# Performance work log

Measured on AMD Instinct MI355X. Metric: run time of the kernel, lower is better.

The kernel has to match this reference:

```python
import jax, jax.numpy as jnp
import numpy as np

B, N, D = 16, 2048, 64


def setup_inputs() -> dict:
    key = jax.random.key(0)
    kq, kk, kv = jax.random.split(key, 3)
    queries = jax.random.normal(kq, (B, N, D), dtype=jnp.float32)
    keys = jax.random.normal(kk, (B, N, D), dtype=jnp.float32)
    values = jax.random.normal(kv, (B, N, D), dtype=jnp.float32)
    return {"queries": queries, "keys": keys, "values": values}


def reference(queries, keys, values):
    d = queries.shape[-1]
    scale = 1.0 / jnp.sqrt(jnp.asarray(d, dtype=queries.dtype))
    # scores: [B, N, N] = Q @ K^T / sqrt(d)
    scores = jnp.einsum("bqd,bkd->bqk", queries, keys) * scale
    attn = jax.nn.softmax(scores, axis=-1)
    # dropout prob = 0.0 -> identity (inference-faithful)
    out = jnp.einsum("bqk,bkd->bqd", attn, values)
    return out
```

## Files before the change

kernel.cpp:

```cpp
#include <hip/hip_runtime.h>

typedef __attribute__((ext_vector_type(8)))  __bf16 bf16x8;
typedef __attribute__((ext_vector_type(16))) float  f32x16;
typedef __attribute__((ext_vector_type(4)))  float  f32x4;

#define B_    16
#define N_    2048
#define D_    64
#define QBLK  128
#define KVBLK 32
#define NT    (N_ / KVBLK)
#define NG    4
#define TPG   (NT / NG)

#define VSTR    80
#define KSZ     4096
#define SLOT_SZ (KSZ + 64 * VSTR)
#define GRP_SZ  (2 * SLOT_SZ)
#define SMEM_SZ (NG * GRP_SZ)

static __device__ __forceinline__ float fast_exp2(float x) {
#if __has_builtin(__builtin_amdgcn_exp2f)
    return __builtin_amdgcn_exp2f(x);
#else
    return __expf(x * 0.6931471805599453f);
#endif
}

__global__ __attribute__((amdgpu_waves_per_eu(4, 4))) __launch_bounds__(1024)
void attn_fwd(const float* __restrict__ Qp, const float* __restrict__ Kp,
              const float* __restrict__ Vp, float* __restrict__ Op)
{
    __shared__ __align__(16) char smem[SMEM_SZ];

    const int tid  = threadIdx.x;
    const int g    = tid >> 8;
    const int tg   = tid & 255;
    const int lane = tid & 63;
    const int w    = (tid >> 6) & 3;
    const int h    = lane >> 5;
    const int qcol = lane & 31;

    const int bx    = blockIdx.x;
    const int batch = ((bx & 7) << 1) | ((bx >> 3) & 1);
    const int qtile = bx >> 4;
    const int q0w   = qtile * QBLK + w * 32;

    const float SL2E = 0.18033688011112042f;
    const size_t bboff = (size_t)batch * (N_ * D_);
    char* gbase = smem + g * GRP_SZ;

    const float* qrow = Qp + bboff + (size_t)(q0w + qcol) * D_ + h * 8;
    bf16x8 qf[4];
#pragma unroll
    for (int m = 0; m < 4; ++m) {
        f32x4 a = *reinterpret_cast<const f32x4*>(qrow + m * 16);
        f32x4 b = *reinterpret_cast<const f32x4*>(qrow + m * 16 + 4);
#pragma unroll
        for (int j = 0; j < 4; ++j) {
            qf[m][j]     = (__bf16)(a[j] * SL2E);
            qf[m][4 + j] = (__bf16)(b[j] * SL2E);
        }
    }

    const int krow = tg >> 3,  kcol = (tg & 7) * 8;
    const int vrow = tg & 31,  vcol = (tg >> 5) * 8;
    const int vin  = vrow & 15;
    const int vpos = ((vrow >> 4) * 2 + ((vin >> 2) & 1)) * 8 + (vin & 3) + 4 * (vin >> 3);
    const float* ksrc0 = Kp + bboff + (size_t)krow * D_ + kcol;
    const float* vsrc0 = Vp + bboff + (size_t)vrow * D_ + vcol;

    f32x4 kr[2], vr[2];
    auto load_tile = [&](int t) {
        const float* ks = ksrc0 + (size_t)t * KVBLK * D_;
        const float* vs = vsrc0 + (size_t)t * KVBLK * D_;
        kr[0] = *reinterpret_cast<const f32x4*>(ks);
        kr[1] = *reinterpret_cast<const f32x4*>(ks + 4);
        vr[0] = *reinterpret_cast<const f32x4*>(vs);
        vr[1] = *reinterpret_cast<const f32x4*>(vs + 4);
    };

    auto write_tile = [&](int b) {
        char* kb = gbase + b * SLOT_SZ;
        char* vb = kb + KSZ;
        bf16x8 w0;
#pragma unroll
        for (int j = 0; j < 4; ++j) { w0[j] = (__bf16)kr[0][j]; w0[4 + j] = (__bf16)kr[1][j]; }
        *reinterpret_cast<bf16x8*>(kb + krow * 128 + ((kcol * 2) ^ ((krow & 7) << 4))) = w0;
#pragma unroll 8
        for (int i = 0; i < 8; ++i) {
            const int d = vcol + i;
            *reinterpret_cast<__bf16*>(vb + d * VSTR + vpos * 2) =
                (__bf16)vr[i >> 2][i & 3];
        }
    };

    f32x16 o0, o1;
#pragma unroll
    for (int i = 0; i < 16; ++i) { o0[i] = 0.f; o1[i] = 0.f; }
    float l_run = 0.f;

    const int kx = (qcol & 7) << 4;

    load_tile(g);
    write_tile(0);
    __syncthreads();

    for (int it = 0; it < TPG; ++it) {
        const int cur = it & 1;
        if (it + 1 < TPG) load_tile(NG * (it + 1) + g);

        const char* kb = gbase + cur * SLOT_SZ;
        const char* vb = kb + KSZ;

        f32x16 s;
#pragma unroll
        for (int i = 0; i < 16; ++i) s[i] = 0.f;
        __builtin_amdgcn_s_setprio(1);
#pragma unroll
        for (int m = 0; m < 4; ++m) {
            const int col = m * 32 + h * 16;
            bf16x8 k0 = *reinterpret_cast<const bf16x8*>(kb + qcol * 128 + (col ^ kx));
            s = __builtin_amdgcn_mfma_f32_32x32x16_bf16(k0, qf[m], s, 0, 0, 0);
        }
        __builtin_amdgcn_s_setprio(0);

        float ps0 = 0.f, ps1 = 0.f, ps2 = 0.f, ps3 = 0.f;
        bf16x8 pfa, pfb;
#pragma unroll
        for (int i = 0; i < 4; ++i) {
            float p0 = fast_exp2(s[i]);
            float p1 = fast_exp2(s[4 + i]);
            float p2 = fast_exp2(s[8 + i]);
            float p3 = fast_exp2(s[12 + i]);
            ps0 += p0; ps1 += p1; ps2 += p2; ps3 += p3;
            pfa[i] = (__bf16)p0; pfa[4 + i] = (__bf16)p1;
            pfb[i] = (__bf16)p2; pfb[4 + i] = (__bf16)p3;
        }
        l_run += (ps0 + ps1) + (ps2 + ps3);

        if (it + 1 < TPG) write_tile(cur ^ 1);

        __builtin_amdgcn_s_setprio(1);
#pragma unroll
        for (int db = 0; db < 2; ++db) {
            const char* vrowp = vb + (db * 32 + qcol) * VSTR + h * 16;
            f32x16& oo = db ? o1 : o0;
#pragma unroll
            for (int sub = 0; sub < 2; ++sub) {
                bf16x8 vf = *reinterpret_cast<const bf16x8*>(vrowp + sub * 32);
                oo = __builtin_amdgcn_mfma_f32_32x32x16_bf16(vf, sub ? pfb : pfa, oo, 0, 0, 0);
            }
        }
        __builtin_amdgcn_s_setprio(0);

        __syncthreads();
    }

    float lt = l_run + __shfl_xor(l_run, 32);
    float* mlF  = (float*)smem;
    float* slab = (float*)smem;
    const int q  = w * 32 + qcol;

    if (h == 0) mlF[g * QBLK + q] = lt;
    __syncthreads();

    const float L = mlF[0 * QBLK + q] + mlF[1 * QBLK + q]
                  + mlF[2 * QBLK + q] + mlF[3 * QBLK + q];
    const float inv = 1.0f / L;
    __syncthreads();

    const int dl0 = 4 * h;
    auto slab_write = [&](float* sb, const f32x16& oo, int db) {
#pragma unroll
        for (int r = 0; r < 16; ++r) {
            const int d = db * 32 + (r & 3) + 8 * (r >> 2) + dl0;
            sb[d * 128 + q] = oo[r];
        }
    };
    auto slab_add = [&](const float* sb, f32x16& oo, int db) {
#pragma unroll
        for (int r = 0; r < 16; ++r) {
            const int d = db * 32 + (r & 3) + 8 * (r >> 2) + dl0;
            oo[r] += sb[d * 128 + q];
        }
    };

    if (g == 1) { slab_write(slab, o0, 0);        slab_write(slab, o1, 1); }
    if (g == 3) { slab_write(slab + 8192, o0, 0); slab_write(slab + 8192, o1, 1); }
    __syncthreads();

    if (g == 0) { slab_add(slab, o0, 0);        slab_add(slab, o1, 1); }
    if (g == 2) { slab_add(slab + 8192, o0, 0); slab_add(slab + 8192, o1, 1); }
    __syncthreads();

    if (g == 2) { slab_write(slab, o0, 0); slab_write(slab, o1, 1); }
    __syncthreads();

    if (g == 0) {
#pragma unroll
        for (int r = 0; r < 16; ++r) {
            const int d0 = (r & 3) + 8 * (r >> 2) + dl0;
            o0[r] = (o0[r] + slab[d0 * 128 + q]) * inv;
            o1[r] = (o1[r] + slab[(32 + d0) * 128 + q]) * inv;
        }
        float* orow = Op + bboff + (size_t)(q0w + qcol) * D_;
#pragma unroll
        for (int gg8 = 0; gg8 < 4; ++gg8) {
            f32x4 v, v2;
#pragma unroll
            for (int r = 0; r < 4; ++r) { v[r] = o0[4 * gg8 + r]; v2[r] = o1[4 * gg8 + r]; }
            *reinterpret_cast<f32x4*>(orow + gg8 * 8 + 4 * h)      = v;
            *reinterpret_cast<f32x4*>(orow + 32 + gg8 * 8 + 4 * h) = v2;
        }
    }
}

extern "C" void kernel_launch(void* const* d_in, const int* in_sizes, int n_in,
                              void* d_out, int out_size, void* d_ws, size_t ws_size,
                              hipStream_t stream) {
    const float* Q = (const float*)d_in[0];
    const float* K = (const float*)d_in[1];
    const float* V = (const float*)d_in[2];
    float* O = (float*)d_out;
    dim3 grid(256), block(1024);
    hipLaunchKernelGGL(attn_fwd, grid, block, 0, stream, Q, K, V, O);
}
```

Baseline: 37.11 us.

## Process 64-row KV tiles as two 32-row phases per barrier

Doubles the KV tile per loop iteration to 64 rows, processed as two 32-row sub-phases, each with its own global prefetch and LDS write into the next buffer. This halves the number of __syncthreads barriers per group and keeps the per-phase register footprint unchanged. In exchange LDS use doubles, to roughly 147 KB, and some code is duplicated; an unused helper lambda is left behind.

```diff
diff --git a/kernel.cpp b/kernel.cpp
--- a/kernel.cpp
+++ b/kernel.cpp
@@ -8,14 +8,15 @@
 #define N_    2048
 #define D_    64
 #define QBLK  128
-#define KVBLK 32
+#define KVBLK 64
 #define NT    (N_ / KVBLK)
 #define NG    4
 #define TPG   (NT / NG)
 
 #define VSTR    80
-#define KSZ     4096
-#define SLOT_SZ (KSZ + 64 * VSTR)
+#define KSZ     8192
+#define VASZ    5120
+#define SLOT_SZ (KSZ + 2 * VASZ)
 #define GRP_SZ  (2 * SLOT_SZ)
 #define SMEM_SZ (NG * GRP_SZ)
 
@@ -71,22 +72,24 @@
     const float* vsrc0 = Vp + bboff + (size_t)vrow * D_ + vcol;
 
     f32x4 kr[2], vr[2];
-    auto load_tile = [&](int t) {
-        const float* ks = ksrc0 + (size_t)t * KVBLK * D_;
-        const float* vs = vsrc0 + (size_t)t * KVBLK * D_;
+    auto load_phase = [&](int t, int ph) {
+        const size_t off = ((size_t)t * KVBLK + ph * 32) * D_;
+        const float* ks = ksrc0 + off;
+        const float* vs = vsrc0 + off;
         kr[0] = *reinterpret_cast<const f32x4*>(ks);
         kr[1] = *reinterpret_cast<const f32x4*>(ks + 4);
         vr[0] = *reinterpret_cast<const f32x4*>(vs);
         vr[1] = *reinterpret_cast<const f32x4*>(vs + 4);
     };
 
-    auto write_tile = [&](int b) {
+    auto write_phase = [&](int b, int ph) {
         char* kb = gbase + b * SLOT_SZ;
-        char* vb = kb + KSZ;
+        char* vb = kb + KSZ + ph * VASZ;
         bf16x8 w0;
 #pragma unroll
         for (int j = 0; j < 4; ++j) { w0[j] = (__bf16)kr[0][j]; w0[4 + j] = (__bf16)kr[1][j]; }
-        *reinterpret_cast<bf16x8*>(kb + krow * 128 + ((kcol * 2) ^ ((krow & 7) << 4))) = w0;
+        *reinterpret_cast<bf16x8*>(kb + (ph * 32 + krow) * 128 +
+                                   ((kcol * 2) ^ ((krow & 7) << 4))) = w0;
 #pragma unroll 8
         for (int i = 0; i < 8; ++i) {
             const int d = vcol + i;
@@ -102,17 +105,7 @@
 
     const int kx = (qcol & 7) << 4;
 
-    load_tile(g);
-    write_tile(0);
-    __syncthreads();
-
-    for (int it = 0; it < TPG; ++it) {
-        const int cur = it & 1;
-        if (it + 1 < TPG) load_tile(NG * (it + 1) + g);
-
-        const char* kb = gbase + cur * SLOT_SZ;
-        const char* vb = kb + KSZ;
-
+    auto sub_half = [&](const char* kb, int sub) {
         f32x16 s;
 #pragma unroll
         for (int i = 0; i < 16; ++i) s[i] = 0.f;
@@ -120,7 +113,8 @@
 #pragma unroll
         for (int m = 0; m < 4; ++m) {
             const int col = m * 32 + h * 16;
-            bf16x8 k0 = *reinterpret_cast<const bf16x8*>(kb + qcol * 128 + (col ^ kx));
+            bf16x8 k0 = *reinterpret_cast<const bf16x8*>(
+                kb + (sub * 32 + qcol) * 128 + (col ^ kx));
             s = __builtin_amdgcn_mfma_f32_32x32x16_bf16(k0, qf[m], s, 0, 0, 0);
         }
         __builtin_amdgcn_s_setprio(0);
@@ -139,23 +133,123 @@
         }
         l_run += (ps0 + ps1) + (ps2 + ps3);
 
-        if (it + 1 < TPG) write_tile(cur ^ 1);
-
+        const char* vb = kb + KSZ + sub * VASZ;
         __builtin_amdgcn_s_setprio(1);
 #pragma unroll
         for (int db = 0; db < 2; ++db) {
             const char* vrowp = vb + (db * 32 + qcol) * VSTR + h * 16;
             f32x16& oo = db ? o1 : o0;
 #pragma unroll
-            for (int sub = 0; sub < 2; ++sub) {
-                bf16x8 vf = *reinterpret_cast<const bf16x8*>(vrowp + sub * 32);
-                oo = __builtin_amdgcn_mfma_f32_32x32x16_bf16(vf, sub ? pfb : pfa, oo, 0, 0, 0);
+            for (int sc = 0; sc < 2; ++sc) {
+                bf16x8 vf = *reinterpret_cast<const bf16x8*>(vrowp + sc * 32);
+                oo = __builtin_amdgcn_mfma_f32_32x32x16_bf16(vf, sc ? pfb : pfa, oo, 0, 0, 0);
             }
         }
         __builtin_amdgcn_s_setprio(0);
-
+    };
+
+    load_phase(g, 0);  write_phase(0, 0);
+    load_phase(g, 1);  write_phase(0, 1);
+    __syncthreads();
+
+    for (int it = 0; it < TPG; ++it) {
+        const int cur = it & 1;
+        const int nxt = cur ^ 1;
+        const bool more = (it + 1 < TPG);
+        const int tn = NG * (it + 1) + g;
+        const char* kb = gbase + cur * SLOT_SZ;
+
+        if (more) load_phase(tn, 0);
+        {
+            f32x16 s;
+#pragma unroll
+            for (int i = 0; i < 16; ++i) s[i] = 0.f;
+            __builtin_amdgcn_s_setprio(1);
+#pragma unroll
+            for (int m = 0; m < 4; ++m) {
+                const int col = m * 32 + h * 16;
+                bf16x8 k0 = *reinterpret_cast<const bf16x8*>(kb + qcol * 128 + (col ^ kx));
+                s = __builtin_amdgcn_mfma_f32_32x32x16_bf16(k0, qf[m], s, 0, 0, 0);
+            }
+            __builtin_amdgcn_s_setprio(0);
+            float ps0 = 0.f, ps1 = 0.f, ps2 = 0.f, ps3 = 0.f;
+            bf16x8 pfa, pfb;
+#pragma unroll
+            for (int i = 0; i < 4; ++i) {
+                float p0 = fast_exp2(s[i]);
+                float p1 = fast_exp2(s[4 + i]);
+                float p2 = fast_exp2(s[8 + i]);
+                float p3 = fast_exp2(s[12 + i]);
+                ps0 += p0; ps1 += p1; ps2 += p2; ps3 += p3;
+                pfa[i] = (__bf16)p0; pfa[4 + i] = (__bf16)p1;
+                pfb[i] = (__bf16)p2; pfb[4 + i] = (__bf16)p3;
+            }
+            l_run += (ps0 + ps1) + (ps2 + ps3);
+
+            if (more) write_phase(nxt, 0);
+
+            const char* vb = kb + KSZ;
+            __builtin_amdgcn_s_setprio(1);
+#pragma unroll
+            for (int db = 0; db < 2; ++db) {
+                const char* vrowp = vb + (db * 32 + qcol) * VSTR + h * 16;
+                f32x16& oo = db ? o1 : o0;
+#pragma unroll
+                for (int sc = 0; sc < 2; ++sc) {
+                    bf16x8 vf = *reinterpret_cast<const bf16x8*>(vrowp + sc * 32);
+                    oo = __builtin_amdgcn_mfma_f32_32x32x16_bf16(vf, sc ? pfb : pfa, oo, 0, 0, 0);
+                }
+            }
+            __builtin_amdgcn_s_setprio(0);
+        }
+
+        if (more) load_phase(tn, 1);
+        {
+            f32x16 s;
+#pragma unroll
+            for (int i = 0; i < 16; ++i) s[i] = 0.f;
+            __builtin_amdgcn_s_setprio(1);
+#pragma unroll
+            for (int m = 0; m < 4; ++m) {
+                const int col = m * 32 + h * 16;
+                bf16x8 k0 = *reinterpret_cast<const bf16x8*>(
+                    kb + (32 + qcol) * 128 + (col ^ kx));
+                s = __builtin_amdgcn_mfma_f32_32x32x16_bf16(k0, qf[m], s, 0, 0, 0);
+            }
+            __builtin_amdgcn_s_setprio(0);
+            float ps0 = 0.f, ps1 = 0.f, ps2 = 0.f, ps3 = 0.f;
+            bf16x8 pfa, pfb;
+#pragma unroll
+            for (int i = 0; i < 4; ++i) {
+                float p0 = fast_exp2(s[i]);
+                float p1 = fast_exp2(s[4 + i]);
+                float p2 = fast_exp2(s[8 + i]);
+                float p3 = fast_exp2(s[12 + i]);
+                ps0 += p0; ps1 += p1; ps2 += p2; ps3 += p3;
+                pfa[i] = (__bf16)p0; pfa[4 + i] = (__bf16)p1;
+                pfb[i] = (__bf16)p2; pfb[4 + i] = (__bf16)p3;
+            }
+            l_run += (ps0 + ps1) + (ps2 + ps3);
+
+            if (more) write_phase(nxt, 1);
+
+            const char* vb = kb + KSZ + VASZ;
+            __builtin_amdgcn_s_setprio(1);
+#pragma unroll
+            for (int db = 0; db < 2; ++db) {
+                const char* vrowp = vb + (db * 32 + qcol) * VSTR + h * 16;
+                f32x16& oo = db ? o1 : o0;
+#pragma unroll
+                for (int sc = 0; sc < 2; ++sc) {
+                    bf16x8 vf = *reinterpret_cast<const bf16x8*>(vrowp + sc * 32);
+                    oo = __builtin_amdgcn_mfma_f32_32x32x16_bf16(vf, sc ? pfb : pfa, oo, 0, 0, 0);
+                }
+            }
+            __builtin_amdgcn_s_setprio(0);
+        }
         __syncthreads();
     }
+    (void)sub_half;
 
     float lt = l_run + __shfl_xor(l_run, 32);
     float* mlF  = (float*)smem;
```

After: 35.90 us. 1.03x faster.
